# Performance work log

Measured on AMD Instinct MI355X. Metric: run time of the kernel, lower is better.

Reference implementation:

```python
import jax, jax.numpy as jnp
import numpy as np

P = 3   # patch_size
D = 7   # displacement window side (odd)
K = 4   # top-k
C = 32  # n_feat
B, H, W = 2, 64, 64
EPS = 1e-12  # F.normalize default eps


def _unfold(x, p):
    """torch F.unfold(x, p, padding=p//2) -> [b, c, p*p, h, w] (row-major patch offsets)."""
    b, c, h, w = x.shape
    pad = p // 2
    xp = jnp.pad(x, ((0, 0), (0, 0), (pad, pad), (pad, pad)))
    return jnp.stack([xp[:, :, i:i + h, j:j + w] for i in range(p) for j in range(p)], axis=2)


def setup_inputs() -> dict:
    key = jax.random.key(0)
    ks = jax.random.split(key, 6)
    feat_t = jax.random.normal(ks[0], (B, C, H, W), jnp.float32)
    feat_tm1 = jax.random.normal(ks[1], (B, C, H, W), jnp.float32)
    # aggregator: Conv2d(k, 1, 1) == weighted sum over k + bias
    agg_w = jax.random.normal(ks[2], (K,), jnp.float32) / K
    agg_b = jax.random.normal(ks[3], (), jnp.float32) * 0.01
    # w_proj: Conv2d(2c, c*p^2, 1) == pointwise linear
    wproj_w = jax.random.normal(ks[4], (C * P * P, 2 * C), jnp.float32) / np.sqrt(2 * C)
    wproj_b = jax.random.normal(ks[5], (C * P * P,), jnp.float32) * 0.01
    return dict(feat_t=feat_t, feat_tm1=feat_tm1, agg_w=agg_w, agg_b=agg_b,
                wproj_w=wproj_w, wproj_b=wproj_b)


def reference(feat_t, feat_tm1, agg_w, agg_b, wproj_w, wproj_b):
    b, c, h, w = feat_t.shape
    p2, d2 = P * P, D * D
    # 3x3 patch unfold of both frames -> [b, c*9, h, w]
    ft_u = _unfold(feat_t, P).reshape(b, c * p2, h, w)
    ftm1_u = _unfold(feat_tm1, P).reshape(b, c * p2, h, w)
    # displacement window over previous-frame patches -> [b, c*9, h, w, d^2]
    disp = jnp.moveaxis(_unfold(ftm1_u, D), 2, -1)
    # cosine similarity along the (c*9) descriptor axis
    ft_n = ft_u / jnp.maximum(jnp.linalg.norm(ft_u, axis=1, keepdims=True), EPS)
    dot = jnp.einsum('bchw,bchwd->bhwd', ft_n, disp)          # [b,h,w,d2]
    dnorm = jnp.maximum(jnp.linalg.norm(disp, axis=1), EPS)    # [b,h,w,d2]
    sim = dot / dnorm
    # top-k displacements per pixel, gather their patch descriptors
    _, idx = jax.lax.top_k(sim, K)                             # [b,h,w,K]
    idx_b = jnp.broadcast_to(idx[:, None], (b, c * p2, h, w, K))
    rel = jnp.take_along_axis(disp, idx_b, axis=-1)            # [b, c*9, h, w, K]
    rel = rel.reshape(b, c, p2, h, w, K)
    # aggregator 1x1 conv over k -> [b, c, h, w, p2]
    agg = jnp.einsum('bcphwk,k->bchwp', rel, agg_w) + agg_b
    # per-pixel patch weights from concatenated features
    cat = jnp.concatenate([feat_t, feat_tm1], axis=1)          # [b, 2c, h, w]
    wgt = jnp.einsum('bihw,oi->bohw', cat, wproj_w) + wproj_b[None, :, None, None]
    wgt = jnp.moveaxis(wgt.reshape(b, c, p2, h, w), 2, -1)     # [b, c, h, w, p2]
    return jnp.sum(agg * wgt, axis=-1)                         # [b, c, h, w]
```

## Files before the change

### kernel.cpp

```cpp
#include <hip/hip_runtime.h>

constexpr float EPSF = 1e-12f;

using short8 = __attribute__((ext_vector_type(8))) short;
using f32x4  = __attribute__((ext_vector_type(4))) float;

__device__ __forceinline__ unsigned short f2bf(float f) {
    unsigned int u = __float_as_uint(f);
    u += 0x7fffu + ((u >> 16) & 1u);
    return (unsigned short)(u >> 16);
}

__global__ __launch_bounds__(512, 4) void agg_mono(
    const float* __restrict__ ft, const float* __restrict__ f1,
    const float* __restrict__ agg_w, const float* __restrict__ agg_bp,
    const float* __restrict__ wproj_w, const float* __restrict__ wproj_b,
    float* __restrict__ out)
{
    __shared__ __align__(16) float pool[16254];
    __shared__ int chosb[16][4];

    float* qw   = pool;
    float* kw   = pool + 1944;
    float* wgtl = pool + 9720;
    float* Tb   = pool + 14904;
    float* Nb   = pool + 15884;
    float* rbnb = pool + 16100;
    unsigned short* Wb = reinterpret_cast<unsigned short*>(pool);
    unsigned short* Bb = reinterpret_cast<unsigned short*>(pool + 14392);

    const int t = threadIdx.x;
    const int pix0 = blockIdx.x << 4;
    const int b  = pix0 >> 12;
    const int y  = (pix0 >> 6) & 63;
    const int x0 = pix0 & 63;

    const float* ftb = ft + ((size_t)b << 17);
    const float* f1b = f1 + ((size_t)b << 17);

    float stgK[14];
    #pragma unroll
    for (int s = 0; s < 14; ++s) {
        int idx = (s << 9) + t;
        if (idx < 6912) {
            int c = idx / 216, rem = idx - c * 216;
            int kr = rem / 24, kc = rem - kr * 24;
            int gy = y - 4 + kr, gx = x0 - 4 + kc;
            stgK[s] = ((unsigned)gy < 64u && (unsigned)gx < 64u)
                    ? f1b[((size_t)c << 12) + (gy << 6) + gx] : 0.f;
        }
    }
    float stgQ[4];
    #pragma unroll
    for (int s = 0; s < 4; ++s) {
        int idx = (s << 9) + t;
        if (idx < 1728) {
            int c = idx / 54, rem = idx - c * 54;
            int qr = rem / 18, qc = rem - qr * 18;
            int gy = y - 1 + qr, gx = x0 - 1 + qc;
            stgQ[s] = ((unsigned)gy < 64u && (unsigned)gx < 64u)
                    ? ftb[((size_t)c << 12) + (gy << 6) + gx] : 0.f;
        }
    }

    #pragma unroll
    for (int s = 0; s < 2; ++s) {
        int idx = (s << 9) + t;
        int i = idx >> 4, ppx = idx & 15;
        const float* src = (i < 32) ? ftb : f1b;
        float v = src[((size_t)(i & 31) << 12) + (y << 6) + x0 + ppx];
        Bb[(((i >> 3) << 4) + ppx) * 8 + (i & 7)] = f2bf(v);
    }

    {
        const float4* w4g = reinterpret_cast<const float4*>(wproj_w);
        #pragma unroll
        for (int s = 0; s < 9; ++s) {
            int f4 = (s << 9) + t;
            float4 wv = w4g[f4];
            int o = f4 >> 4, k4 = f4 & 15;
            int off = ((((o >> 4) << 3) + (k4 >> 1)) * 16 + (o & 15)) * 8
                    + ((k4 & 1) << 2);
            ushort4 bv;
            bv.x = f2bf(wv.x); bv.y = f2bf(wv.y);
            bv.z = f2bf(wv.z); bv.w = f2bf(wv.w);
            *reinterpret_cast<ushort4*>(&Wb[off]) = bv;
        }
    }
    __syncthreads();

    {
        const int lane = t & 63;
        const int wv8 = t >> 6;
        const int lr = lane & 15;
        const int lg = lane >> 4;
        short8 bf0 = *reinterpret_cast<const short8*>(&Bb[(lg * 16 + lr) * 8]);
        short8 bf1 = *reinterpret_cast<const short8*>(&Bb[((4 + lg) * 16 + lr) * 8]);
        #pragma unroll
        for (int ti = 0; ti < 3; ++ti) {
            if (ti == 2 && wv8 >= 2) break;
            const int tt = (ti == 0) ? wv8 : (ti == 1 ? wv8 + 8 : wv8 + 16);
            const float4 bias = *reinterpret_cast<const float4*>(
                wproj_b + tt * 16 + lg * 4);
            f32x4 acc;
            acc[0] = bias.x; acc[1] = bias.y; acc[2] = bias.z; acc[3] = bias.w;
            short8 a0 = *reinterpret_cast<const short8*>(
                &Wb[((tt * 8 + lg) * 16 + lr) * 8]);
            short8 a1 = *reinterpret_cast<const short8*>(
                &Wb[((tt * 8 + 4 + lg) * 16 + lr) * 8]);
            acc = __builtin_amdgcn_mfma_f32_16x16x32_bf16(a0, bf0, acc, 0, 0, 0);
            acc = __builtin_amdgcn_mfma_f32_16x16x32_bf16(a1, bf1, acc, 0, 0, 0);
            *reinterpret_cast<f32x4*>(&wgtl[lr * 292 + tt * 16 + lg * 4]) = acc;
        }
    }
    __syncthreads();

    #pragma unroll
    for (int s = 0; s < 14; ++s) {
        int idx = (s << 9) + t;
        if (idx < 6912) {
            int c = idx / 216, rem = idx - c * 216;
            kw[rem * 36 + c] = stgK[s];
        }
    }
    #pragma unroll
    for (int s = 0; s < 4; ++s) {
        int idx = (s << 9) + t;
        if (idx < 1728) {
            int c = idx / 54, rem = idx - c * 54;
            qw[rem * 36 + c] = stgQ[s];
        }
    }
    __syncthreads();

    if (t < 216) {
        float s = 0.f;
        #pragma unroll
        for (int c4 = 0; c4 < 8; ++c4) {
            float4 v = *reinterpret_cast<const float4*>(&kw[t * 36 + (c4 << 2)]);
            s += v.x * v.x + v.y * v.y + v.z * v.z + v.w * v.w;
        }
        Nb[t] = s;
    }
    __syncthreads();
    if (t < 154) {
        int cyi = t / 22, cxi = t - cyi * 22;
        int kr = cyi + 1, kc = cxi + 1;
        float bn = 0.f;
        #pragma unroll
        for (int di = -1; di <= 1; ++di)
            #pragma unroll
            for (int dj = -1; dj <= 1; ++dj)
                bn += Nb[(kr + di) * 24 + kc + dj];
        rbnb[t] = 1.0f / fmaxf(sqrtf(bn), EPSF);
    }

    {
        const int g = t >> 3, c4 = t & 7;
        #pragma unroll
        for (int pr = 0; pr < 2; ++pr) {
            int p = (pr << 6) + g;
            if (p < 126) {
                int u = p / 18, xx = p - u * 18;
                float av[7] = {0.f, 0.f, 0.f, 0.f, 0.f, 0.f, 0.f};
                #pragma unroll
                for (int r = 0; r < 3; ++r) {
                    float4 qv = *reinterpret_cast<const float4*>(
                        &qw[(r * 18 + xx) * 36 + (c4 << 2)]);
                    #pragma unroll
                    for (int v = 0; v < 7; ++v) {
                        float4 kv = *reinterpret_cast<const float4*>(
                            &kw[((r + u) * 24 + xx + v) * 36 + (c4 << 2)]);
                        av[v] += qv.x * kv.x + qv.y * kv.y + qv.z * kv.z + qv.w * kv.w;
                    }
                }
                #pragma unroll
                for (int v = 0; v < 7; ++v) {
                    float s = av[v];
                    s += __shfl_xor(s, 1, 64);
                    s += __shfl_xor(s, 2, 64);
                    s += __shfl_xor(s, 4, 64);
                    if (c4 == 0) Tb[(u * 7 + v) * 20 + xx] = s;
                }
            }
        }
    }
    __syncthreads();

    {
        const int lane = t & 63;
        const int wvv = t >> 6;
        const int hf = lane >> 5;
        const int c = lane & 31;
        const int ppx = (wvv << 1) + hf;
        float s0 = 0.f, s1;
        {
            int u = c / 7, v = c - u * 7;
            int cy = y + u - 3, cx = x0 + ppx + v - 3;
            if ((unsigned)cy < 64u && (unsigned)cx < 64u) {
                float dot = Tb[c * 20 + ppx] + Tb[c * 20 + ppx + 1]
                          + Tb[c * 20 + ppx + 2];
                s0 = dot * rbnb[u * 22 + ppx + v];
            }
        }
        if (c < 17) {
            int d = c + 32;
            int u = d / 7, v = d - u * 7;
            int cy = y + u - 3, cx = x0 + ppx + v - 3;
            s1 = 0.f;
            if ((unsigned)cy < 64u && (unsigned)cx < 64u) {
                float dot = Tb[d * 20 + ppx] + Tb[d * 20 + ppx + 1]
                          + Tb[d * 20 + ppx + 2];
                s1 = dot * rbnb[u * 22 + ppx + v];
            }
        } else s1 = -3.0e38f;
        #pragma unroll
        for (int k = 0; k < 4; ++k) {
            float bs; int bi;
            if (s0 >= s1) { bs = s0; bi = c; }
            else          { bs = s1; bi = c + 32; }
            #pragma unroll
            for (int off = 16; off; off >>= 1) {
                float os = __shfl_xor(bs, off, 64);
                int   oi = __shfl_xor(bi, off, 64);
                if (os > bs || (os == bs && oi < bi)) { bs = os; bi = oi; }
            }
            if (c == 0) chosb[ppx][k] = bi;
            if (bi == c)           s0 = -3.0e38f;
            else if (bi == c + 32) s1 = -3.0e38f;
        }
    }
    __syncthreads();

    {
        const int px = t & 15;
        const int c  = t >> 4;
        const float ab = agg_bp[0];
        float awv[4];
        #pragma unroll
        for (int k = 0; k < 4; ++k) awv[k] = agg_w[k];
        int uo[4], vo[4]; bool cval[4];
        #pragma unroll
        for (int k = 0; k < 4; ++k) {
            int d = chosb[px][k];
            int u = d / 7, v = d - u * 7;
            int cy = y + u - 3, cx = x0 + px + v - 3;
            cval[k] = ((unsigned)cy < 64u) && ((unsigned)cx < 64u);
            uo[k] = u; vo[k] = v;
        }
        float outv = 0.f;
        #pragma unroll
        for (int j = 0; j < 9; ++j) {
            int pi = j / 3, pj = j - pi * 3;
            float gacc = ab;
            #pragma unroll
            for (int k = 0; k < 4; ++k) {
                float vv = cval[k]
                    ? kw[((uo[k] + pi) * 24 + px + vo[k] + pj) * 36 + c] : 0.f;
                gacc += awv[k] * vv;
            }
            outv += wgtl[px * 292 + c * 9 + j] * gacc;
        }
        out[((size_t)((b << 5) + c) << 12) + (y << 6) + x0 + px] = outv;
    }
}

extern "C" void kernel_launch(void* const* d_in, const int* in_sizes, int n_in,
                              void* d_out, int out_size, void* d_ws, size_t ws_size,
                              hipStream_t stream)
{
    const float* feat_t   = (const float*)d_in[0];
    const float* feat_tm1 = (const float*)d_in[1];
    const float* agg_w    = (const float*)d_in[2];
    const float* agg_b    = (const float*)d_in[3];
    const float* wproj_w  = (const float*)d_in[4];
    const float* wproj_b  = (const float*)d_in[5];
    float* outp = (float*)d_out;
    (void)d_ws; (void)ws_size;

    agg_mono<<<512, 512, 0, stream>>>(feat_t, feat_tm1, agg_w, agg_b,
                                      wproj_w, wproj_b, outp);
}
```

Measured before the change: 22.38 us.

## Restructure staging, load weights directly into MFMA regs, reuse K rows in correlation

Removes the shared-memory staging of wproj weights. Each wave now loads its bf16 A fragments straight from global memory, which lets the register staging plus one barrier phase be dropped and K/Q be written to LDS as float4 over 4 channels. The correlation loop is reorganised so each loaded K row is reused across three query rows. The rbnb normalisation now runs concurrently on otherwise idle threads. The final aggregation uses 128 threads that each handle 4 channels with float4 LDS reads and a transposed wgt layout. The occupancy hint in launch_bounds is removed, which may change register allocation.

```diff
diff --git a/kernel.cpp b/kernel.cpp
--- a/kernel.cpp
+++ b/kernel.cpp
@@ -11,22 +11,21 @@
     return (unsigned short)(u >> 16);
 }
 
-__global__ __launch_bounds__(512, 4) void agg_mono(
+__global__ __launch_bounds__(512) void agg_mono(
     const float* __restrict__ ft, const float* __restrict__ f1,
     const float* __restrict__ agg_w, const float* __restrict__ agg_bp,
     const float* __restrict__ wproj_w, const float* __restrict__ wproj_b,
     float* __restrict__ out)
 {
-    __shared__ __align__(16) float pool[16254];
+    __shared__ __align__(16) float pool[15742];
     __shared__ int chosb[16][4];
 
     float* qw   = pool;
     float* kw   = pool + 1944;
     float* wgtl = pool + 9720;
-    float* Tb   = pool + 14904;
-    float* Nb   = pool + 15884;
-    float* rbnb = pool + 16100;
-    unsigned short* Wb = reinterpret_cast<unsigned short*>(pool);
+    float* Tb   = pool + 14392;
+    float* Nb   = pool + 15372;
+    float* rbnb = pool + 15588;
     unsigned short* Bb = reinterpret_cast<unsigned short*>(pool + 14392);
 
     const int t = threadIdx.x;
@@ -38,54 +37,39 @@
     const float* ftb = ft + ((size_t)b << 17);
     const float* f1b = f1 + ((size_t)b << 17);
 
-    float stgK[14];
-    #pragma unroll
-    for (int s = 0; s < 14; ++s) {
-        int idx = (s << 9) + t;
-        if (idx < 6912) {
-            int c = idx / 216, rem = idx - c * 216;
-            int kr = rem / 24, kc = rem - kr * 24;
-            int gy = y - 4 + kr, gx = x0 - 4 + kc;
-            stgK[s] = ((unsigned)gy < 64u && (unsigned)gx < 64u)
-                    ? f1b[((size_t)c << 12) + (gy << 6) + gx] : 0.f;
-        }
-    }
-    float stgQ[4];
     #pragma unroll
     for (int s = 0; s < 4; ++s) {
         int idx = (s << 9) + t;
         if (idx < 1728) {
-            int c = idx / 54, rem = idx - c * 54;
-            int qr = rem / 18, qc = rem - qr * 18;
-            int gy = y - 1 + qr, gx = x0 - 1 + qc;
-            stgQ[s] = ((unsigned)gy < 64u && (unsigned)gx < 64u)
-                    ? ftb[((size_t)c << 12) + (gy << 6) + gx] : 0.f;
-        }
-    }
-
+            int c4 = idx / 216, pos = idx - c4 * 216;
+            int kr = pos / 24, kc = pos - kr * 24;
+            int gy = y - 4 + kr, gx = x0 - 4 + kc;
+            float4 v = {0.f, 0.f, 0.f, 0.f};
+            if ((unsigned)gy < 64u && (unsigned)gx < 64u) {
+                const float* p = f1b + ((size_t)(c4 << 2) << 12) + (gy << 6) + gx;
+                v.x = p[0]; v.y = p[1 << 12]; v.z = p[2 << 12]; v.w = p[3 << 12];
+            }
+            *reinterpret_cast<float4*>(&kw[pos * 36 + (c4 << 2)]) = v;
+        }
+    }
+    if (t < 432) {
+        int c4 = t / 54, pos = t - c4 * 54;
+        int qr = pos / 18, qc = pos - qr * 18;
+        int gy = y - 1 + qr, gx = x0 - 1 + qc;
+        float4 v = {0.f, 0.f, 0.f, 0.f};
+        if ((unsigned)gy < 64u && (unsigned)gx < 64u) {
+            const float* p = ftb + ((size_t)(c4 << 2) << 12) + (gy << 6) + gx;
+            v.x = p[0]; v.y = p[1 << 12]; v.z = p[2 << 12]; v.w = p[3 << 12];
+        }
+        *reinterpret_cast<float4*>(&qw[pos * 36 + (c4 << 2)]) = v;
+    }
     #pragma unroll
     for (int s = 0; s < 2; ++s) {
         int idx = (s << 9) + t;
-        int i = idx >> 4, ppx = idx & 15;
+        int i = idx >> 4, px16 = idx & 15;
         const float* src = (i < 32) ? ftb : f1b;
-        float v = src[((size_t)(i & 31) << 12) + (y << 6) + x0 + ppx];
-        Bb[(((i >> 3) << 4) + ppx) * 8 + (i & 7)] = f2bf(v);
-    }
-
-    {
-        const float4* w4g = reinterpret_cast<const float4*>(wproj_w);
-        #pragma unroll
-        for (int s = 0; s < 9; ++s) {
-            int f4 = (s << 9) + t;
-            float4 wv = w4g[f4];
-            int o = f4 >> 4, k4 = f4 & 15;
-            int off = ((((o >> 4) << 3) + (k4 >> 1)) * 16 + (o & 15)) * 8
-                    + ((k4 & 1) << 2);
-            ushort4 bv;
-            bv.x = f2bf(wv.x); bv.y = f2bf(wv.y);
-            bv.z = f2bf(wv.z); bv.w = f2bf(wv.w);
-            *reinterpret_cast<ushort4*>(&Wb[off]) = bv;
-        }
+        float v = src[((size_t)(i & 31) << 12) + (y << 6) + x0 + px16];
+        Bb[(((i >> 3) << 4) + px16) * 8 + (i & 7)] = f2bf(v);
     }
     __syncthreads();
 
@@ -100,39 +84,34 @@
         for (int ti = 0; ti < 3; ++ti) {
             if (ti == 2 && wv8 >= 2) break;
             const int tt = (ti == 0) ? wv8 : (ti == 1 ? wv8 + 8 : wv8 + 16);
+            const float* wrow = wproj_w + (size_t)(tt * 16 + lr) * 64 + lg * 8;
+            float4 wa = *reinterpret_cast<const float4*>(wrow);
+            float4 wb = *reinterpret_cast<const float4*>(wrow + 4);
+            float4 wc = *reinterpret_cast<const float4*>(wrow + 32);
+            float4 wd = *reinterpret_cast<const float4*>(wrow + 36);
+            short8 a0, a1;
+            a0[0] = (short)f2bf(wa.x); a0[1] = (short)f2bf(wa.y);
+            a0[2] = (short)f2bf(wa.z); a0[3] = (short)f2bf(wa.w);
+            a0[4] = (short)f2bf(wb.x); a0[5] = (short)f2bf(wb.y);
+            a0[6] = (short)f2bf(wb.z); a0[7] = (short)f2bf(wb.w);
+            a1[0] = (short)f2bf(wc.x); a1[1] = (short)f2bf(wc.y);
+            a1[2] = (short)f2bf(wc.z); a1[3] = (short)f2bf(wc.w);
+            a1[4] = (short)f2bf(wd.x); a1[5] = (short)f2bf(wd.y);
+            a1[6] = (short)f2bf(wd.z); a1[7] = (short)f2bf(wd.w);
             const float4 bias = *reinterpret_cast<const float4*>(
                 wproj_b + tt * 16 + lg * 4);
             f32x4 acc;
             acc[0] = bias.x; acc[1] = bias.y; acc[2] = bias.z; acc[3] = bias.w;
-            short8 a0 = *reinterpret_cast<const short8*>(
-                &Wb[((tt * 8 + lg) * 16 + lr) * 8]);
-            short8 a1 = *reinterpret_cast<const short8*>(
-                &Wb[((tt * 8 + 4 + lg) * 16 + lr) * 8]);
             acc = __builtin_amdgcn_mfma_f32_16x16x32_bf16(a0, bf0, acc, 0, 0, 0);
             acc = __builtin_amdgcn_mfma_f32_16x16x32_bf16(a1, bf1, acc, 0, 0, 0);
-            *reinterpret_cast<f32x4*>(&wgtl[lr * 292 + tt * 16 + lg * 4]) = acc;
-        }
-    }
-    __syncthreads();
-
-    #pragma unroll
-    for (int s = 0; s < 14; ++s) {
-        int idx = (s << 9) + t;
-        if (idx < 6912) {
-            int c = idx / 216, rem = idx - c * 216;
-            kw[rem * 36 + c] = stgK[s];
-        }
-    }
-    #pragma unroll
-    for (int s = 0; s < 4; ++s) {
-        int idx = (s << 9) + t;
-        if (idx < 1728) {
-            int c = idx / 54, rem = idx - c * 54;
-            qw[rem * 36 + c] = stgQ[s];
-        }
-    }
-    __syncthreads();
-
+            #pragma unroll
+            for (int qi = 0; qi < 4; ++qi) {
+                int o = tt * 16 + lg * 4 + qi;
+                int c = o / 9, j = o - c * 9;
+                wgtl[lr * 292 + j * 32 + c] = acc[qi];
+            }
+        }
+    }
     if (t < 216) {
         float s = 0.f;
         #pragma unroll
@@ -143,47 +122,64 @@
         Nb[t] = s;
     }
     __syncthreads();
-    if (t < 154) {
-        int cyi = t / 22, cxi = t - cyi * 22;
-        int kr = cyi + 1, kc = cxi + 1;
-        float bn = 0.f;
-        #pragma unroll
-        for (int di = -1; di <= 1; ++di)
-            #pragma unroll
-            for (int dj = -1; dj <= 1; ++dj)
-                bn += Nb[(kr + di) * 24 + kc + dj];
-        rbnb[t] = 1.0f / fmaxf(sqrtf(bn), EPSF);
-    }
-
-    {
-        const int g = t >> 3, c4 = t & 7;
-        #pragma unroll
-        for (int pr = 0; pr < 2; ++pr) {
-            int p = (pr << 6) + g;
-            if (p < 126) {
-                int u = p / 18, xx = p - u * 18;
-                float av[7] = {0.f, 0.f, 0.f, 0.f, 0.f, 0.f, 0.f};
-                #pragma unroll
-                for (int r = 0; r < 3; ++r) {
-                    float4 qv = *reinterpret_cast<const float4*>(
-                        &qw[(r * 18 + xx) * 36 + (c4 << 2)]);
+
+    if (t < 288) {
+        const int vh = (t >= 144) ? 1 : 0;
+        const int tl = t - vh * 144;
+        const int xx = tl >> 3;
+        const int c4 = tl & 7;
+        const int v0 = vh << 2;
+        const int co = c4 << 2;
+        const float4 q0 = *reinterpret_cast<const float4*>(&qw[(     xx) * 36 + co]);
+        const float4 q1 = *reinterpret_cast<const float4*>(&qw[(18 + xx) * 36 + co]);
+        const float4 q2 = *reinterpret_cast<const float4*>(&qw[(36 + xx) * 36 + co]);
+        float acc[7][4];
+        #pragma unroll
+        for (int u = 0; u < 7; ++u)
+            #pragma unroll
+            for (int v = 0; v < 4; ++v) acc[u][v] = 0.f;
+        #pragma unroll
+        for (int a = 0; a < 9; ++a) {
+            float4 ka[4];
+            #pragma unroll
+            for (int v = 0; v < 4; ++v)
+                ka[v] = *reinterpret_cast<const float4*>(
+                    &kw[(a * 24 + xx + v0 + v) * 36 + co]);
+            #pragma unroll
+            for (int r = 0; r < 3; ++r) {
+                if (r <= a && a - r <= 6) {
+                    const float4 qv = (r == 0) ? q0 : (r == 1) ? q1 : q2;
+                    const int u = a - r;
                     #pragma unroll
-                    for (int v = 0; v < 7; ++v) {
-                        float4 kv = *reinterpret_cast<const float4*>(
-                            &kw[((r + u) * 24 + xx + v) * 36 + (c4 << 2)]);
-                        av[v] += qv.x * kv.x + qv.y * kv.y + qv.z * kv.z + qv.w * kv.w;
-                    }
+                    for (int v = 0; v < 4; ++v)
+                        acc[u][v] += qv.x * ka[v].x + qv.y * ka[v].y
+                                   + qv.z * ka[v].z + qv.w * ka[v].w;
                 }
-                #pragma unroll
-                for (int v = 0; v < 7; ++v) {
-                    float s = av[v];
+            }
+        }
+        #pragma unroll
+        for (int u = 0; u < 7; ++u)
+            #pragma unroll
+            for (int v = 0; v < 4; ++v) {
+                if (v0 + v < 7) {
+                    float s = acc[u][v];
                     s += __shfl_xor(s, 1, 64);
                     s += __shfl_xor(s, 2, 64);
                     s += __shfl_xor(s, 4, 64);
-                    if (c4 == 0) Tb[(u * 7 + v) * 20 + xx] = s;
+                    if (c4 == 0) Tb[(u * 7 + v0 + v) * 20 + xx] = s;
                 }
             }
-        }
+    } else if (t < 288 + 154) {
+        const int t2 = t - 288;
+        int cyi = t2 / 22, cxi = t2 - cyi * 22;
+        int kr = cyi + 1, kc = cxi + 1;
+        float bn = 0.f;
+        #pragma unroll
+        for (int di = -1; di <= 1; ++di)
+            #pragma unroll
+            for (int dj = -1; dj <= 1; ++dj)
+                bn += Nb[(kr + di) * 24 + kc + dj];
+        rbnb[t2] = 1.0f / fmaxf(sqrtf(bn), EPSF);
     }
     __syncthreads();
 
@@ -232,9 +228,10 @@
     }
     __syncthreads();
 
-    {
+    if (t < 128) {
         const int px = t & 15;
-        const int c  = t >> 4;
+        const int c4 = t >> 4;
+        const int co = c4 << 2;
         const float ab = agg_bp[0];
         float awv[4];
         #pragma unroll
@@ -248,20 +245,30 @@
             cval[k] = ((unsigned)cy < 64u) && ((unsigned)cx < 64u);
             uo[k] = u; vo[k] = v;
         }
-        float outv = 0.f;
+        float4 outv = {0.f, 0.f, 0.f, 0.f};
         #pragma unroll
         for (int j = 0; j < 9; ++j) {
             int pi = j / 3, pj = j - pi * 3;
-            float gacc = ab;
+            float4 g = {ab, ab, ab, ab};
             #pragma unroll
             for (int k = 0; k < 4; ++k) {
-                float vv = cval[k]
-                    ? kw[((uo[k] + pi) * 24 + px + vo[k] + pj) * 36 + c] : 0.f;
-                gacc += awv[k] * vv;
-            }
-            outv += wgtl[px * 292 + c * 9 + j] * gacc;
-        }
-        out[((size_t)((b << 5) + c) << 12) + (y << 6) + x0 + px] = outv;
+                if (cval[k]) {
+                    float4 vv = *reinterpret_cast<const float4*>(
+                        &kw[((uo[k] + pi) * 24 + px + vo[k] + pj) * 36 + co]);
+                    g.x += awv[k] * vv.x; g.y += awv[k] * vv.y;
+                    g.z += awv[k] * vv.z; g.w += awv[k] * vv.w;
+                }
+            }
+            float4 wg = *reinterpret_cast<const float4*>(
+                &wgtl[px * 292 + j * 32 + co]);
+            outv.x += wg.x * g.x; outv.y += wg.y * g.y;
+            outv.z += wg.z * g.z; outv.w += wg.w * g.w;
+        }
+        const size_t obase = ((size_t)((b << 5) + co) << 12) + (y << 6) + x0 + px;
+        out[obase]              = outv.x;
+        out[obase + (1u << 12)] = outv.y;
+        out[obase + (2u << 12)] = outv.z;
+        out[obase + (3u << 12)] = outv.w;
     }
 }
 
```

Result: slower. 30.14 us (+34.7%).
